# Kernel optimization log

Measured on AMD Instinct MI355X. Metric: run time of the kernel, lower is better.

## Reference

```python
import jax, jax.numpy as jnp
import numpy as np

B, S, D = 4, 512, 768
NH, DH = 12, 64
EXP_N, INV_N = 32, 64


def _scalar_mlp(x, w1, b1, w2, b2):
    # elementwise 1 -> N -> 1 MLP: y = relu(x*w1 + b1) @ w2 + b2, applied per element
    h = jax.nn.relu(x[..., None] * w1 + b1)          # [..., N]
    return jnp.einsum('...n,n->...', h, w2) + b2[0]  # [...]


def fit_softmax(X, exp_w1, exp_b1, exp_w2, exp_b2, inv_w1, inv_b1, inv_w2, inv_b2):
    # X: [B, H, S, S]. Faithful to torch fit_softmax: reference value is X[:, :, 0]
    tmax = X[:, :, 0][..., None]                      # [B, H, S, 1]
    tp = jnp.minimum(X - (tmax - 1.0), 3.0)           # clamp tp > 3 -> 3
    exp_val = _scalar_mlp(tp, exp_w1, exp_b1, exp_w2, exp_b2)
    X_up = jnp.where(tp > -20.0, exp_val, 0.0)        # only index tp > -20
    partition = jnp.sum(X_up, axis=-1, keepdims=True)  # [B, H, S, 1]
    p_inv = _scalar_mlp(partition, inv_w1, inv_b1, inv_w2, inv_b2)
    out = X_up * p_inv
    partition_p2 = jnp.sum(out, axis=-1, keepdims=True)
    p_inv2 = _scalar_mlp(partition_p2, inv_w1, inv_b1, inv_w2, inv_b2)
    # renormalize only rows whose partition exceeds 1.5
    return jnp.where(partition_p2 > 1.5, out * p_inv2, out)


def setup_inputs() -> dict:
    key = jax.random.key(0)
    ks = jax.random.split(key, 16)
    f = jax.random.normal
    return {
        'hidden_states': f(ks[0], (B, S, D), jnp.float32),
        'attention_mask': jnp.zeros((B, 1, 1, S), jnp.float32),
        'Wq': f(ks[1], (D, D), jnp.float32) * 0.02,
        'bq': f(ks[2], (D,), jnp.float32) * 0.02,
        'Wk': f(ks[3], (D, D), jnp.float32) * 0.02,
        'bk': f(ks[4], (D,), jnp.float32) * 0.02,
        'Wv': f(ks[5], (D, D), jnp.float32) * 0.02,
        'bv': f(ks[6], (D,), jnp.float32) * 0.02,
        'exp_w1': f(ks[7], (EXP_N,), jnp.float32),
        'exp_b1': f(ks[8], (EXP_N,), jnp.float32),
        'exp_w2': f(ks[9], (EXP_N,), jnp.float32) * 0.1,
        'exp_b2': f(ks[10], (1,), jnp.float32) * 0.1,
        'inv_w1': f(ks[11], (INV_N,), jnp.float32),
        'inv_b1': f(ks[12], (INV_N,), jnp.float32),
        'inv_w2': f(ks[13], (INV_N,), jnp.float32) * 0.1,
        'inv_b2': f(ks[14], (1,), jnp.float32) * 0.1,
    }


def reference(hidden_states, attention_mask, Wq, bq, Wk, bk, Wv, bv,
              exp_w1, exp_b1, exp_w2, exp_b2, inv_w1, inv_b1, inv_w2, inv_b2):
    def split_heads(x):  # [B, S, D] -> [B, H, S, DH]
        return x.reshape(B, S, NH, DH).transpose(0, 2, 1, 3)

    q = split_heads(hidden_states @ Wq.T + bq)
    k = split_heads(hidden_states @ Wk.T + bk)
    v = split_heads(hidden_states @ Wv.T + bv)

    scores = jnp.einsum('bhqd,bhkd->bhqk', q, k) / np.float32(np.sqrt(DH))
    scores = scores + attention_mask
    probs = fit_softmax(scores, exp_w1, exp_b1, exp_w2, exp_b2,
                        inv_w1, inv_b1, inv_w2, inv_b2)
    ctx = jnp.einsum('bhqk,bhkd->bhqd', probs, v)     # [B, H, S, DH]
    return ctx.transpose(0, 2, 1, 3).reshape(B, S, D)
```

## Files before the change

### kernel.cpp

```cpp
#include <hip/hip_runtime.h>
#include <math.h>

typedef unsigned short u16;
typedef short bf16x8 __attribute__((ext_vector_type(8)));
typedef float f32x4 __attribute__((ext_vector_type(4)));

#define BN 4
#define SN 512
#define DN 768
#define NHN 12
#define DHN 64
#define EXPN 32
#define INVN 64

#define TAB_T0 -20.5f
#define TAB_DLT (23.5f / 448.0f)
#define TAB_SCALE (448.0f / 23.5f)

__device__ __forceinline__ u16 f2b(float f) {
    union { float f; unsigned int u; } v; v.f = f;
    unsigned int r = v.u + 0x7FFFu + ((v.u >> 16) & 1u);
    return (u16)(r >> 16);
}
__device__ __forceinline__ u16 f2h(float f) {
    union { _Float16 h; u16 u; } v; v.h = (_Float16)f; return v.u;
}

#define GLD16(g, l) __builtin_amdgcn_global_load_lds( \
    (__attribute__((address_space(1))) const void*)(g), \
    (__attribute__((address_space(3))) void*)(l), 16, 0, 0)

__global__ __launch_bounds__(256) void prep(
    const float* __restrict__ X, const float* __restrict__ Wq,
    const float* __restrict__ Wk, const float* __restrict__ Wv,
    const float* __restrict__ ew1, const float* __restrict__ eb1,
    const float* __restrict__ ew2, const float* __restrict__ eb2,
    u16* __restrict__ Xb, u16* __restrict__ Wqb,
    u16* __restrict__ Wkb, u16* __restrict__ Wvb,
    float2* __restrict__ tbl)
{
    if (blockIdx.y == 4) {
        int i = blockIdx.x * 256 + threadIdx.x;
        if (i > 449) return;
        float t0 = TAB_T0 + i * TAB_DLT;
        float t1 = t0 + TAB_DLT;
        float y0 = eb2[0], y1 = y0;
        #pragma unroll 8
        for (int n = 0; n < EXPN; ++n) {
            float w1 = ew1[n], b1 = eb1[n], w2 = ew2[n];
            y0 += fmaxf(fmaf(t0, w1, b1), 0.f) * w2;
            y1 += fmaxf(fmaf(t1, w1, b1), 0.f) * w2;
        }
        tbl[i] = make_float2(y0, y1 - y0);
        return;
    }
    const float* s; u16* d; int n;
    switch (blockIdx.y) {
        case 0:  s = X;  d = Xb;  n = (BN * SN) * DN; break;
        case 1:  s = Wq; d = Wqb; n = DN * DN; break;
        case 2:  s = Wk; d = Wkb; n = DN * DN; break;
        default: s = Wv; d = Wvb; n = DN * DN; break;
    }
    int i = (blockIdx.x * 256 + threadIdx.x) * 4;
    if (i < n) {
        float4 v = *(const float4*)&s[i];
        unsigned int lo = (unsigned)f2b(v.x) | ((unsigned)f2b(v.y) << 16);
        unsigned int hi = (unsigned)f2b(v.z) | ((unsigned)f2b(v.w) << 16);
        *(uint2*)&d[i] = make_uint2(lo, hi);
    }
}

__global__ __launch_bounds__(256) void qkv_mfma(
    const u16* __restrict__ Xb,
    const u16* __restrict__ Wqb, const u16* __restrict__ Wkb, const u16* __restrict__ Wvb,
    const float* __restrict__ bq, const float* __restrict__ bk, const float* __restrict__ bv,
    u16* __restrict__ Qb, u16* __restrict__ Kb, u16* __restrict__ Vtr)
{
    __shared__ __align__(16) u16 As[128 * 32];
    __shared__ __align__(16) u16 Bs[64 * 32];

    const int tid = threadIdx.x, w = tid >> 6, l = tid & 63;
    const int lr = l & 15, lg = l >> 4;
    const int m0 = blockIdx.y * 128;
    const int nsel = blockIdx.x / 12;
    const int n0l = (blockIdx.x % 12) * 64;
    const u16* W = (nsel == 0) ? Wqb : (nsel == 1) ? Wkb : Wvb;
    const float* bias = (nsel == 0) ? bq : (nsel == 1) ? bk : bv;

    const int wm = w >> 1, wn = w & 1;

    const int oA0 = tid * 16;
    const int rA0 = oA0 >> 6, sA0 = (oA0 >> 4) & 3;
    const int cA0 = (sA0 ^ ((rA0 >> 1) & 3)) * 8;
    const int oA1 = oA0 + 4096;
    const int rA1 = oA1 >> 6, sA1 = (oA1 >> 4) & 3;
    const int cA1 = (sA1 ^ ((rA1 >> 1) & 3)) * 8;
    const u16* gA0 = Xb + (m0 + rA0) * DN + cA0;
    const u16* gA1 = Xb + (m0 + rA1) * DN + cA1;
    const u16* gB  = W + (n0l + rA0) * DN + cA0;

    int offA[4], offB[2];
    #pragma unroll
    for (int mi = 0; mi < 4; ++mi) {
        int row = wm * 64 + mi * 16 + lr;
        offA[mi] = row * 64 + ((lg ^ ((row >> 1) & 3)) * 16);
    }
    #pragma unroll
    for (int ni = 0; ni < 2; ++ni) {
        int row = wn * 32 + ni * 16 + lr;
        offB[ni] = row * 64 + ((lg ^ ((row >> 1) & 3)) * 16);
    }

    f32x4 acc[4][2];
    #pragma unroll
    for (int mi = 0; mi < 4; ++mi)
        #pragma unroll
        for (int ni = 0; ni < 2; ++ni) acc[mi][ni] = (f32x4){0.f, 0.f, 0.f, 0.f};

    for (int k0 = 0; k0 < DN; k0 += 32) {
        __syncthreads();
        GLD16(gA0 + k0, (char*)As + oA0);
        GLD16(gA1 + k0, (char*)As + oA1);
        GLD16(gB  + k0, (char*)Bs + oA0);
        __syncthreads();

        bf16x8 af[4], bff[2];
        #pragma unroll
        for (int mi = 0; mi < 4; ++mi) af[mi] = *(const bf16x8*)((const char*)As + offA[mi]);
        #pragma unroll
        for (int ni = 0; ni < 2; ++ni) bff[ni] = *(const bf16x8*)((const char*)Bs + offB[ni]);
        #pragma unroll
        for (int mi = 0; mi < 4; ++mi)
            #pragma unroll
            for (int ni = 0; ni < 2; ++ni)
                acc[mi][ni] = __builtin_amdgcn_mfma_f32_16x16x32_bf16(af[mi], bff[ni], acc[mi][ni], 0, 0, 0);
    }

    if (nsel < 2) {
        u16* out = (nsel == 0) ? Qb : Kb;
        #pragma unroll
        for (int ni = 0; ni < 2; ++ni) {
            int col = n0l + wn * 32 + ni * 16 + lr;
            float bc = bias[col];
            int hh = col >> 6, dh = col & 63;
            #pragma unroll
            for (int mi = 0; mi < 4; ++mi) {
                #pragma unroll
                for (int r = 0; r < 4; ++r) {
                    int m = m0 + wm * 64 + mi * 16 + lg * 4 + r;
                    int bi = m >> 9, srow = m & 511;
                    out[(((bi * NHN + hh) * SN) + srow) * DHN + dh] = f2b(acc[mi][ni][r] + bc);
                }
            }
        }
    } else {
        #pragma unroll
        for (int ni = 0; ni < 2; ++ni) {
            int col = n0l + wn * 32 + ni * 16 + lr;
            float bc = bias[col];
            int hh = col >> 6, dh = col & 63;
            #pragma unroll
            for (int mi = 0; mi < 4; ++mi) {
                int m = m0 + wm * 64 + mi * 16 + lg * 4;
                int bi = m >> 9, srow = m & 511;
                ushort4 pk;
                pk.x = f2h(acc[mi][ni][0] + bc);
                pk.y = f2h(acc[mi][ni][1] + bc);
                pk.z = f2h(acc[mi][ni][2] + bc);
                pk.w = f2h(acc[mi][ni][3] + bc);
                *(ushort4*)&Vtr[((size_t)(bi * NHN + hh) * DHN + dh) * SN + srow] = pk;
            }
        }
    }
}

__global__ __launch_bounds__(512, 6) void attn_mfma(
    const u16* __restrict__ Qb, const u16* __restrict__ Kb, const u16* __restrict__ Vtr,
    const float* __restrict__ mask, const float2* __restrict__ tbl,
    const float* __restrict__ iw1, const float* __restrict__ ib1,
    const float* __restrict__ iw2, const float* __restrict__ ib2,
    float* __restrict__ out)
{
    __shared__ __align__(16) u16 sb[32 * 512];
    __shared__ __align__(16) float2 tab[450];
    __shared__ float ms[SN];
    __shared__ float wI1[INVN], wIb1[INVN], wI2[INVN];
    __shared__ float partw[8][32];
    __shared__ float scale_s[32];
    __shared__ float scal;

    const int tid = threadIdx.x, w = tid >> 6, l = tid & 63;
    const int lr = l & 15, lg = l >> 4, kb8 = lg * 8;
    const int bid = blockIdx.x;
    const int bh = bid >> 4;
    const int q0 = (bid & 15) * 32;
    const int b = bh / NHN, h = bh % NHN;
    const u16* Qh = Qb + (size_t)bh * SN * DHN;
    const u16* Kh = Kb + (size_t)bh * SN * DHN;
    const u16* VTh = Vtr + (size_t)bh * DHN * SN;

    if (tid < INVN) { wI1[tid] = iw1[tid]; wIb1[tid] = ib1[tid]; wI2[tid] = iw2[tid]; }
    if (tid == 511) scal = ib2[0];
    if (tid < SN) ms[tid] = mask[b * SN + tid];
    if (tid < 450) tab[tid] = tbl[tid];
    __syncthreads();

    const float ib2v = scal;

    bf16x8 aq00 = *(const bf16x8*)(Qh + (q0 + lr) * DHN + kb8);
    bf16x8 aq01 = *(const bf16x8*)(Qh + (q0 + lr) * DHN + 32 + kb8);
    bf16x8 aq10 = *(const bf16x8*)(Qh + (q0 + 16 + lr) * DHN + kb8);
    bf16x8 aq11 = *(const bf16x8*)(Qh + (q0 + 16 + lr) * DHN + 32 + kb8);

    float myref0[4], myref1[4];
    {
        bf16x8 a00 = *(const bf16x8*)(Qh + kb8);
        bf16x8 a01 = *(const bf16x8*)(Qh + 32 + kb8);
        const u16* kp0 = Kh + (q0 + lr) * DHN + kb8;
        bf16x8 b00 = *(const bf16x8*)(kp0);
        bf16x8 b01 = *(const bf16x8*)(kp0 + 32);
        const u16* kp1 = Kh + (q0 + 16 + lr) * DHN + kb8;
        bf16x8 b10 = *(const bf16x8*)(kp1);
        bf16x8 b11 = *(const bf16x8*)(kp1 + 32);
        f32x4 d0 = {0.f, 0.f, 0.f, 0.f}, d1 = {0.f, 0.f, 0.f, 0.f};
        d0 = __builtin_amdgcn_mfma_f32_16x16x32_bf16(a00, b00, d0, 0, 0, 0);
        d0 = __builtin_amdgcn_mfma_f32_16x16x32_bf16(a01, b01, d0, 0, 0, 0);
        d1 = __builtin_amdgcn_mfma_f32_16x16x32_bf16(a00, b10, d1, 0, 0, 0);
        d1 = __builtin_amdgcn_mfma_f32_16x16x32_bf16(a01, b11, d1, 0, 0, 0);
        float rc0 = d0[0] * 0.125f + ms[q0 + lr];
        float rc1 = d1[0] * 0.125f + ms[q0 + 16 + lr];
        #pragma unroll
        for (int r = 0; r < 4; ++r) {
            myref0[r] = __shfl(rc0, lg * 4 + r);
            myref1[r] = __shfl(rc1, lg * 4 + r);
        }
    }

    char* sbb = (char*)sb;
    float part0[4] = {0.f, 0.f, 0.f, 0.f};
    float part1[4] = {0.f, 0.f, 0.f, 0.f};
    const u16* kpp = Kh + (w * 64 + lr) * DHN + kb8;
    bf16x8 nb0 = *(const bf16x8*)(kpp);
    bf16x8 nb1 = *(const bf16x8*)(kpp + 32);
    #pragma unroll
    for (int i = 0; i < 4; ++i) {
        bf16x8 b0 = nb0, b1 = nb1;
        if (i < 3) {
            const u16* kn = kpp + (i + 1) * 16 * DHN;
            nb0 = *(const bf16x8*)(kn);
            nb1 = *(const bf16x8*)(kn + 32);
        }
        f32x4 d0 = {0.f, 0.f, 0.f, 0.f}, d1 = {0.f, 0.f, 0.f, 0.f};
        __builtin_amdgcn_s_setprio(1);
        d0 = __builtin_amdgcn_mfma_f32_16x16x32_bf16(aq00, b0, d0, 0, 0, 0);
        d0 = __builtin_amdgcn_mfma_f32_16x16x32_bf16(aq01, b1, d0, 0, 0, 0);
        d1 = __builtin_amdgcn_mfma_f32_16x16x32_bf16(aq10, b0, d1, 0, 0, 0);
        d1 = __builtin_amdgcn_mfma_f32_16x16x32_bf16(aq11, b1, d1, 0, 0, 0);
        __builtin_amdgcn_s_setprio(0);
        const int col0 = w * 64 + i * 16;
        const float mv = ms[col0 + lr];
        const int colb = (col0 + lr) * 2;
        #pragma unroll
        for (int r = 0; r < 4; ++r) {
            {
                float tp = fminf(d0[r] * 0.125f + mv - (myref0[r] - 1.0f), 3.0f);
                float v = (tp - TAB_T0) * TAB_SCALE;
                int idx = (int)v;
                idx = idx < 0 ? 0 : idx;
                float fr = v - (float)idx;
                float2 p = tab[idx];
                float e = fmaf(fr, p.y, p.x);
                float xu = (tp > -20.0f) ? e : 0.f;
                part0[r] += xu;
                int row = lg * 4 + r;
                *(u16*)(sbb + row * 1024 + (colb ^ ((row & 7) << 4))) = f2h(xu);
            }
            {
                float tp = fminf(d1[r] * 0.125f + mv - (myref1[r] - 1.0f), 3.0f);
                float v = (tp - TAB_T0) * TAB_SCALE;
                int idx = (int)v;
                idx = idx < 0 ? 0 : idx;
                float fr = v - (float)idx;
                float2 p = tab[idx];
                float e = fmaf(fr, p.y, p.x);
                float xu = (tp > -20.0f) ? e : 0.f;
                part1[r] += xu;
                int row = 16 + lg * 4 + r;
                *(u16*)(sbb + row * 1024 + (colb ^ ((row & 7) << 4))) = f2h(xu);
            }
        }
    }
    #pragma unroll
    for (int r = 0; r < 4; ++r) {
        #pragma unroll
        for (int s = 1; s < 16; s <<= 1) {
            part0[r] += __shfl_xor(part0[r], s);
            part1[r] += __shfl_xor(part1[r], s);
        }
    }
    if (lr == 0) {
        #pragma unroll
        for (int r = 0; r < 4; ++r) {
            partw[w][lg * 4 + r] = part0[r];
            partw[w][16 + lg * 4 + r] = part1[r];
        }
    }
    __syncthreads();

    #pragma unroll
    for (int rr = 0; rr < 4; ++rr) {
        const int row = w * 4 + rr;
        float pt = 0.f;
        #pragma unroll
        for (int ww = 0; ww < 8; ++ww) pt += partw[ww][row];
        float hu = fmaxf(fmaf(pt, wI1[l], wIb1[l]), 0.f) * wI2[l];
        #pragma unroll
        for (int s = 32; s > 0; s >>= 1) hu += __shfl_xor(hu, s);
        const float pinv = hu + ib2v;
        const float p2 = pt * pinv;
        float hu2 = fmaxf(fmaf(p2, wI1[l], wIb1[l]), 0.f) * wI2[l];
        #pragma unroll
        for (int s = 32; s > 0; s >>= 1) hu2 += __shfl_xor(hu2, s);
        const float pinv2 = hu2 + ib2v;
        if (l == 0) scale_s[row] = pinv * ((p2 > 1.5f) ? pinv2 : 1.0f);
    }

    const int ds = (w & 3) * 16, kh = w >> 2;
    f32x4 acc0 = {0.f, 0.f, 0.f, 0.f}, acc1 = {0.f, 0.f, 0.f, 0.f};
    const u16* vp = VTh + (ds + lr) * SN + kh * 256 + kb8;
    const int swzl = (lr & 7) << 4;
    bf16x8 nv = *(const bf16x8*)(vp);
    #pragma unroll
    for (int k0 = 0; k0 < 256; k0 += 32) {
        bf16x8 bv = nv;
        if (k0 < 224) nv = *(const bf16x8*)(vp + k0 + 32);
        const int kk2 = (kh * 256 + k0 + kb8) * 2;
        bf16x8 a0 = *(const bf16x8*)(sbb + lr * 1024 + (kk2 ^ swzl));
        bf16x8 a1 = *(const bf16x8*)(sbb + (16 + lr) * 1024 + (kk2 ^ swzl));
        __builtin_amdgcn_s_setprio(1);
        acc0 = __builtin_amdgcn_mfma_f32_16x16x32_f16(a0, bv, acc0, 0, 0, 0);
        acc1 = __builtin_amdgcn_mfma_f32_16x16x32_f16(a1, bv, acc1, 0, 0, 0);
        __builtin_amdgcn_s_setprio(0);
    }
    float (*pvbuf)[68] = (float (*)[68])sbb;
    __syncthreads();
    if (kh == 1) {
        #pragma unroll
        for (int r = 0; r < 4; ++r) {
            pvbuf[lg * 4 + r][ds + lr] = acc0[r];
            pvbuf[16 + lg * 4 + r][ds + lr] = acc1[r];
        }
    }
    __syncthreads();
    if (kh == 0) {
        #pragma unroll
        for (int r = 0; r < 4; ++r) {
            const int row0 = lg * 4 + r;
            const int row1 = row0 + 16;
            float v0 = (acc0[r] + pvbuf[row0][ds + lr]) * scale_s[row0];
            float v1 = (acc1[r] + pvbuf[row1][ds + lr]) * scale_s[row1];
            out[(size_t)(b * SN + q0 + row0) * DN + h * DHN + ds + lr] = v0;
            out[(size_t)(b * SN + q0 + row1) * DN + h * DHN + ds + lr] = v1;
        }
    }
}

extern "C" void kernel_launch(void* const* d_in, const int* in_sizes, int n_in,
                              void* d_out, int out_size, void* d_ws, size_t ws_size,
                              hipStream_t stream) {
    const float* X    = (const float*)d_in[0];
    const float* mask = (const float*)d_in[1];
    const float* Wq   = (const float*)d_in[2];
    const float* bq   = (const float*)d_in[3];
    const float* Wk   = (const float*)d_in[4];
    const float* bk   = (const float*)d_in[5];
    const float* Wv   = (const float*)d_in[6];
    const float* bv   = (const float*)d_in[7];
    const float* ew1  = (const float*)d_in[8];
    const float* eb1  = (const float*)d_in[9];
    const float* ew2  = (const float*)d_in[10];
    const float* eb2  = (const float*)d_in[11];
    const float* iw1  = (const float*)d_in[12];
    const float* ib1  = (const float*)d_in[13];
    const float* iw2  = (const float*)d_in[14];
    const float* ib2  = (const float*)d_in[15];
    float* out = (float*)d_out;

    float2* tbl = (float2*)d_ws;
    u16* Xb  = (u16*)((char*)d_ws + 4608);
    u16* Wqb = Xb + (size_t)(BN * SN) * DN;
    u16* Wkb = Wqb + DN * DN;
    u16* Wvb = Wkb + DN * DN;
    u16* Qb  = Wvb + DN * DN;
    const size_t per = (size_t)BN * NHN * SN * DHN;
    u16* Kb2 = Qb + per;
    u16* Vb2 = Kb2 + per;

    dim3 gc(1536, 5);
    prep<<<gc, 256, 0, stream>>>(X, Wq, Wk, Wv, ew1, eb1, ew2, eb2,
                                 Xb, Wqb, Wkb, Wvb, tbl);

    dim3 g1(36, 16);
    qkv_mfma<<<g1, 256, 0, stream>>>(Xb, Wqb, Wkb, Wvb, bq, bk, bv, Qb, Kb2, Vb2);

    attn_mfma<<<dim3(768), 512, 0, stream>>>(Qb, Kb2, Vb2, mask, tbl,
                                             iw1, ib1, iw2, ib2, out);
}
```

Before: 55.78 us.

## Double QKV GEMM K-tile to 64 and fold softmax reference offset into FMA

The QKV projection GEMM now stages a 64-wide K slice per iteration instead of 32. This halves the number of barrier-separated load iterations and issues two MFMAs per accumulator per stage, using a new 128-byte row XOR swizzle for LDS. The attention kernel precomputes (mask - (ref-1)) per row group so each score costs one fma before the clamp. The larger LDS tiles raise shared memory use per block and may lower occupancy, and the rounding order of the score arithmetic changes slightly.

```diff
diff --git a/kernel.cpp b/kernel.cpp
--- a/kernel.cpp
+++ b/kernel.cpp
@@ -76,8 +76,8 @@
     const float* __restrict__ bq, const float* __restrict__ bk, const float* __restrict__ bv,
     u16* __restrict__ Qb, u16* __restrict__ Kb, u16* __restrict__ Vtr)
 {
-    __shared__ __align__(16) u16 As[128 * 32];
-    __shared__ __align__(16) u16 Bs[64 * 32];
+    __shared__ __align__(16) u16 As[128 * 64];
+    __shared__ __align__(16) u16 Bs[64 * 64];
 
     const int tid = threadIdx.x, w = tid >> 6, l = tid & 63;
     const int lr = l & 15, lg = l >> 4;
@@ -89,26 +89,41 @@
 
     const int wm = w >> 1, wn = w & 1;
 
-    const int oA0 = tid * 16;
-    const int rA0 = oA0 >> 6, sA0 = (oA0 >> 4) & 3;
-    const int cA0 = (sA0 ^ ((rA0 >> 1) & 3)) * 8;
-    const int oA1 = oA0 + 4096;
-    const int rA1 = oA1 >> 6, sA1 = (oA1 >> 4) & 3;
-    const int cA1 = (sA1 ^ ((rA1 >> 1) & 3)) * 8;
-    const u16* gA0 = Xb + (m0 + rA0) * DN + cA0;
-    const u16* gA1 = Xb + (m0 + rA1) * DN + cA1;
-    const u16* gB  = W + (n0l + rA0) * DN + cA0;
-
-    int offA[4], offB[2];
+    const u16* gA[4];
+    int ldsA[4];
+    #pragma unroll
+    for (int i = 0; i < 4; ++i) {
+        int o = i * 4096 + tid * 16;
+        int row = o >> 7, inb = o & 127;
+        int col = (inb ^ ((row & 7) << 4)) >> 1;
+        gA[i] = Xb + (m0 + row) * DN + col;
+        ldsA[i] = o;
+    }
+    const u16* gB[2];
+    int ldsB[2];
+    #pragma unroll
+    for (int i = 0; i < 2; ++i) {
+        int o = i * 4096 + tid * 16;
+        int row = o >> 7, inb = o & 127;
+        int col = (inb ^ ((row & 7) << 4)) >> 1;
+        gB[i] = W + (n0l + row) * DN + col;
+        ldsB[i] = o;
+    }
+
+    int offA[4][2], offB[2][2];
     #pragma unroll
     for (int mi = 0; mi < 4; ++mi) {
         int row = wm * 64 + mi * 16 + lr;
-        offA[mi] = row * 64 + ((lg ^ ((row >> 1) & 3)) * 16);
+        #pragma unroll
+        for (int ks = 0; ks < 2; ++ks)
+            offA[mi][ks] = row * 128 + ((ks * 64 + lg * 16) ^ ((row & 7) << 4));
     }
     #pragma unroll
     for (int ni = 0; ni < 2; ++ni) {
         int row = wn * 32 + ni * 16 + lr;
-        offB[ni] = row * 64 + ((lg ^ ((row >> 1) & 3)) * 16);
+        #pragma unroll
+        for (int ks = 0; ks < 2; ++ks)
+            offB[ni][ks] = row * 128 + ((ks * 64 + lg * 16) ^ ((row & 7) << 4));
     }
 
     f32x4 acc[4][2];
@@ -117,23 +132,32 @@
         #pragma unroll
         for (int ni = 0; ni < 2; ++ni) acc[mi][ni] = (f32x4){0.f, 0.f, 0.f, 0.f};
 
-    for (int k0 = 0; k0 < DN; k0 += 32) {
+    for (int k0 = 0; k0 < DN; k0 += 64) {
         __syncthreads();
-        GLD16(gA0 + k0, (char*)As + oA0);
-        GLD16(gA1 + k0, (char*)As + oA1);
-        GLD16(gB  + k0, (char*)Bs + oA0);
+        #pragma unroll
+        for (int i = 0; i < 4; ++i) GLD16(gA[i] + k0, (char*)As + ldsA[i]);
+        #pragma unroll
+        for (int i = 0; i < 2; ++i) GLD16(gB[i] + k0, (char*)Bs + ldsB[i]);
         __syncthreads();
 
-        bf16x8 af[4], bff[2];
-        #pragma unroll
-        for (int mi = 0; mi < 4; ++mi) af[mi] = *(const bf16x8*)((const char*)As + offA[mi]);
-        #pragma unroll
-        for (int ni = 0; ni < 2; ++ni) bff[ni] = *(const bf16x8*)((const char*)Bs + offB[ni]);
+        bf16x8 af[4][2], bff[2][2];
         #pragma unroll
         for (int mi = 0; mi < 4; ++mi)
             #pragma unroll
-            for (int ni = 0; ni < 2; ++ni)
-                acc[mi][ni] = __builtin_amdgcn_mfma_f32_16x16x32_bf16(af[mi], bff[ni], acc[mi][ni], 0, 0, 0);
+            for (int ks = 0; ks < 2; ++ks)
+                af[mi][ks] = *(const bf16x8*)((const char*)As + offA[mi][ks]);
+        #pragma unroll
+        for (int ni = 0; ni < 2; ++ni)
+            #pragma unroll
+            for (int ks = 0; ks < 2; ++ks)
+                bff[ni][ks] = *(const bf16x8*)((const char*)Bs + offB[ni][ks]);
+        #pragma unroll
+        for (int mi = 0; mi < 4; ++mi)
+            #pragma unroll
+            for (int ni = 0; ni < 2; ++ni) {
+                acc[mi][ni] = __builtin_amdgcn_mfma_f32_16x16x32_bf16(af[mi][0], bff[ni][0], acc[mi][ni], 0, 0, 0);
+                acc[mi][ni] = __builtin_amdgcn_mfma_f32_16x16x32_bf16(af[mi][1], bff[ni][1], acc[mi][ni], 0, 0, 0);
+            }
     }
 
     if (nsel < 2) {
@@ -212,7 +236,7 @@
     bf16x8 aq10 = *(const bf16x8*)(Qh + (q0 + 16 + lr) * DHN + kb8);
     bf16x8 aq11 = *(const bf16x8*)(Qh + (q0 + 16 + lr) * DHN + 32 + kb8);
 
-    float myref0[4], myref1[4];
+    float myref0m1[4], myref1m1[4];
     {
         bf16x8 a00 = *(const bf16x8*)(Qh + kb8);
         bf16x8 a01 = *(const bf16x8*)(Qh + 32 + kb8);
@@ -227,12 +251,12 @@
         d0 = __builtin_amdgcn_mfma_f32_16x16x32_bf16(a01, b01, d0, 0, 0, 0);
         d1 = __builtin_amdgcn_mfma_f32_16x16x32_bf16(a00, b10, d1, 0, 0, 0);
         d1 = __builtin_amdgcn_mfma_f32_16x16x32_bf16(a01, b11, d1, 0, 0, 0);
-        float rc0 = d0[0] * 0.125f + ms[q0 + lr];
-        float rc1 = d1[0] * 0.125f + ms[q0 + 16 + lr];
-        #pragma unroll
-        for (int r = 0; r < 4; ++r) {
-            myref0[r] = __shfl(rc0, lg * 4 + r);
-            myref1[r] = __shfl(rc1, lg * 4 + r);
+        float rc0 = d0[0] * 0.125f + ms[q0 + lr] - 1.0f;
+        float rc1 = d1[0] * 0.125f + ms[q0 + 16 + lr] - 1.0f;
+        #pragma unroll
+        for (int r = 0; r < 4; ++r) {
+            myref0m1[r] = __shfl(rc0, lg * 4 + r);
+            myref1m1[r] = __shfl(rc1, lg * 4 + r);
         }
     }
 
@@ -260,10 +284,16 @@
         const int col0 = w * 64 + i * 16;
         const float mv = ms[col0 + lr];
         const int colb = (col0 + lr) * 2;
+        float mr0[4], mr1[4];
+        #pragma unroll
+        for (int r = 0; r < 4; ++r) {
+            mr0[r] = mv - myref0m1[r];
+            mr1[r] = mv - myref1m1[r];
+        }
         #pragma unroll
         for (int r = 0; r < 4; ++r) {
             {
-                float tp = fminf(d0[r] * 0.125f + mv - (myref0[r] - 1.0f), 3.0f);
+                float tp = fminf(fmaf(d0[r], 0.125f, mr0[r]), 3.0f);
                 float v = (tp - TAB_T0) * TAB_SCALE;
                 int idx = (int)v;
                 idx = idx < 0 ? 0 : idx;
@@ -276,7 +306,7 @@
                 *(u16*)(sbb + row * 1024 + (colb ^ ((row & 7) << 4))) = f2h(xu);
             }
             {
-                float tp = fminf(d1[r] * 0.125f + mv - (myref1[r] - 1.0f), 3.0f);
+                float tp = fminf(fmaf(d1[r], 0.125f, mr1[r]), 3.0f);
                 float v = (tp - TAB_T0) * TAB_SCALE;
                 int idx = (int)v;
                 idx = idx < 0 ? 0 : idx;
```

Result: faster. 52.62 us (-5.7%).
